# Performance work log

Hardware: AMD Instinct MI355X
Metric: run time of the kernel (lower is better)

## Reference

```python
import jax, jax.numpy as jnp
import numpy as np

DIM = 96
HEADS = 6
HEAD_DIM = DIM // HEADS
WIN = 8
N = WIN * WIN           # tokens per window
B_ = 4096               # num_windows * batch
TABLE = (2 * WIN - 1) ** 2  # 225


def setup_inputs() -> dict:
    key = jax.random.key(0)
    ks = jax.random.split(key, 7)
    x = jax.random.normal(ks[0], (B_, N, DIM), dtype=jnp.float32)
    rpi = jax.random.randint(ks[1], (N, N), 0, TABLE)
    qkv_w = jax.random.normal(ks[2], (3 * DIM, DIM), dtype=jnp.float32) * 0.02
    qkv_b = jnp.zeros((3 * DIM,), dtype=jnp.float32)
    proj_w = jax.random.normal(ks[3], (DIM, DIM), dtype=jnp.float32) * 0.02
    proj_b = jnp.zeros((DIM,), dtype=jnp.float32)
    rpb_table = jax.random.normal(ks[4], (TABLE, HEADS), dtype=jnp.float32) * 0.02
    return {"x": x, "rpi": rpi, "qkv_w": qkv_w, "qkv_b": qkv_b,
            "proj_w": proj_w, "proj_b": proj_b, "rpb_table": rpb_table}


def reference(x, rpi, qkv_w, qkv_b, proj_w, proj_b, rpb_table):
    b_, n, c = x.shape
    scale = HEAD_DIM ** -0.5
    # qkv projection: (b_, n, 3, H, hd)
    qkv = (x @ qkv_w.T + qkv_b).reshape(b_, n, 3, HEADS, HEAD_DIM)
    qkv = jnp.transpose(qkv, (2, 0, 3, 1, 4))  # (3, b_, H, n, hd)
    q, k, v = qkv[0], qkv[1], qkv[2]
    attn = jnp.einsum('bhnd,bhmd->bhnm', q * scale, k)
    # relative position bias gather: (n, n, H) -> (H, n, n)
    bias = jnp.transpose(rpb_table[rpi], (2, 0, 1))
    attn = jax.nn.softmax(attn + bias[None], axis=-1)
    out = jnp.einsum('bhnm,bhmd->bnhd', attn, v).reshape(b_, n, c)
    return out @ proj_w.T + proj_b
```

## Files before the change

kernel.cpp:

```cpp
#include <hip/hip_runtime.h>

#define NWIN 4096
#define DIM 96
#define HEADS 6
#define NTOK 64

typedef __bf16 bf16x8 __attribute__((ext_vector_type(8)));
typedef __bf16 bf16x4 __attribute__((ext_vector_type(4)));
typedef float  f32x4  __attribute__((ext_vector_type(4)));

#define WS_QKVW 0
#define WS_PROJW 55296
#define WS_BIAS 73728
#define WS_TOTAL 172032

__device__ __forceinline__ f32x4 mfma16(bf16x8 a, bf16x8 b, f32x4 c) {
  return __builtin_amdgcn_mfma_f32_16x16x32_bf16(a, b, c, 0, 0, 0);
}

__device__ __forceinline__ bf16x8 cvt8(const float* p) {
  const float4* q = (const float4*)p;
  float4 a = q[0];
  float4 b = q[1];
  bf16x8 r;
  r[0] = (__bf16)a.x; r[1] = (__bf16)a.y; r[2] = (__bf16)a.z; r[3] = (__bf16)a.w;
  r[4] = (__bf16)b.x; r[5] = (__bf16)b.y; r[6] = (__bf16)b.z; r[7] = (__bf16)b.w;
  return r;
}

__global__ void prep_kernel(const float* __restrict__ qkv_w,
                            const float* __restrict__ proj_w,
                            const float* __restrict__ rpb,
                            const int* __restrict__ rpi,
                            char* __restrict__ ws) {
  int i = blockIdx.x * blockDim.x + threadIdx.x;
  __bf16* qw = (__bf16*)(ws + WS_QKVW);
  __bf16* pw = (__bf16*)(ws + WS_PROJW);
  float* bias = (float*)(ws + WS_BIAS);
  if (i < 288 * 96) qw[i] = (__bf16)qkv_w[i];
  int j = i - 288 * 96;
  if (j >= 0 && j < 96 * 96) pw[j] = (__bf16)proj_w[j];
  int t = i - (288 * 96 + 96 * 96);
  if (t >= 0 && t < HEADS * 16 * 64 * 4) {
    int r = t & 3;
    int lane = (t >> 2) & 63;
    int ba = (t >> 8) & 15;
    int h = t >> 12;
    int bq = ba >> 2, a = ba & 3;
    int l16 = lane & 15, lq = lane >> 4;
    int qrow = 16 * bq + l16;
    int kcol = 16 * a + 4 * lq + r;
    bias[t] = rpb[rpi[qrow * 64 + kcol] * HEADS + h];
  }
}

template <bool USE_WS>
__global__ __launch_bounds__(384, 8) void win_attn(
    const float* __restrict__ x,
    const int* __restrict__ rpi,
    const float* __restrict__ qkv_w,
    const float* __restrict__ qkv_b,
    const float* __restrict__ proj_w,
    const float* __restrict__ proj_b,
    const float* __restrict__ rpb,
    const char* __restrict__ ws,
    float* __restrict__ out) {
  __shared__ __align__(16) __bf16 lds[22784];

  const int tid = (int)threadIdx.x;
  const int wv = tid >> 6;
  const int lane = tid & 63;
  const int l16 = lane & 15;
  const int lq = lane >> 4;
  const int b = (int)blockIdx.x;

  __bf16* xfrag = lds;
  __bf16* ao = lds;
  __bf16* buf = lds + 6656 + wv * 2688;
  __bf16* vh = buf + 1536;
  __bf16* Pt = vh;

  const float* xw = x + (size_t)b * (NTOK * DIM);
  const __bf16* qwb = (const __bf16*)(ws + WS_QKVW);
  const __bf16* pwb = (const __bf16*)(ws + WS_PROJW);
  const float4* bias4 = (const float4*)(ws + WS_BIAS) + (wv << 10);

  bf16x8 zf = {};

#pragma unroll
  for (int ff = 0; ff < 2; ++ff) {
    const int f = 2 * wv + ff;
    const int mt = f / 3, ks = f - 3 * mt;
    bf16x8 v = cvt8(xw + (16 * mt + l16) * DIM + 32 * ks + 8 * lq);
    *(bf16x8*)(xfrag + (f * 64 + lane) * 8) = v;
  }
  __syncthreads();

#define XV(mt, ks) (*(const bf16x8*)(xfrag + (((mt) * 3 + (ks)) * 64 + lane) * 8))

  {
    const int frow = (HEADS + wv) * 16;
    bf16x8 wb[3];
#pragma unroll
    for (int ks = 0; ks < 3; ++ks) {
      if constexpr (USE_WS)
        wb[ks] = *(const bf16x8*)(qwb + (frow + l16) * 96 + 32 * ks + 8 * lq);
      else
        wb[ks] = cvt8(qkv_w + (frow + l16) * 96 + 32 * ks + 8 * lq);
    }
    const float4 kb4 = *(const float4*)(qkv_b + frow + 4 * lq);
    const float kbv[4] = {kb4.x, kb4.y, kb4.z, kb4.w};
#pragma unroll
    for (int mt = 0; mt < 4; ++mt) {
      f32x4 acc = {0.f, 0.f, 0.f, 0.f};
#pragma unroll
      for (int ks = 0; ks < 3; ++ks) acc = mfma16(wb[ks], XV(mt, ks), acc);
      bf16x4 t;
#pragma unroll
      for (int r = 0; r < 4; ++r) t[r] = (__bf16)(acc[r] + kbv[r]);
      *(bf16x4*)(buf + (16 * mt + l16) * 24 + 4 * lq) = t;
    }
  }
  asm volatile("s_waitcnt lgkmcnt(0)" ::: "memory");

  bf16x8 kb[4];
#pragma unroll
  for (int a = 0; a < 4; ++a)
    kb[a] = (lq < 2) ? *(const bf16x8*)(buf + (16 * a + l16) * 24 + 8 * lq) : zf;

  {
    const int frow = (2 * HEADS + wv) * 16;
    bf16x8 wb[3];
#pragma unroll
    for (int ks = 0; ks < 3; ++ks) {
      if constexpr (USE_WS)
        wb[ks] = *(const bf16x8*)(qwb + (frow + l16) * 96 + 32 * ks + 8 * lq);
      else
        wb[ks] = cvt8(qkv_w + (frow + l16) * 96 + 32 * ks + 8 * lq);
    }
    const float vb = qkv_b[frow + l16];
#pragma unroll
    for (int mt = 0; mt < 4; ++mt) {
      f32x4 acc = {0.f, 0.f, 0.f, 0.f};
#pragma unroll
      for (int ks = 0; ks < 3; ++ks) acc = mfma16(XV(mt, ks), wb[ks], acc);
      bf16x4 t;
#pragma unroll
      for (int r = 0; r < 4; ++r) t[r] = (__bf16)(acc[r] + vb);
      *(bf16x4*)(vh + l16 * 72 + 16 * mt + 4 * lq) = t;
    }
  }
  asm volatile("s_waitcnt lgkmcnt(0)" ::: "memory");

  bf16x8 vbf[2];
#pragma unroll
  for (int c = 0; c < 2; ++c)
    vbf[c] = *(const bf16x8*)(vh + l16 * 72 + 32 * c + 8 * lq);

  {
    const int frow = wv * 16;
    bf16x8 wb[3];
#pragma unroll
    for (int ks = 0; ks < 3; ++ks) {
      if constexpr (USE_WS)
        wb[ks] = *(const bf16x8*)(qwb + (frow + l16) * 96 + 32 * ks + 8 * lq);
      else
        wb[ks] = cvt8(qkv_w + (frow + l16) * 96 + 32 * ks + 8 * lq);
    }
    const float4 qb4 = *(const float4*)(qkv_b + frow + 4 * lq);
    const float qbv[4] = {qb4.x, qb4.y, qb4.z, qb4.w};
#pragma unroll
    for (int mt = 0; mt < 4; ++mt) {
      f32x4 acc = {0.f, 0.f, 0.f, 0.f};
#pragma unroll
      for (int ks = 0; ks < 3; ++ks) acc = mfma16(wb[ks], XV(mt, ks), acc);
      bf16x4 t;
#pragma unroll
      for (int r = 0; r < 4; ++r) t[r] = (__bf16)((acc[r] + qbv[r]) * 0.25f);
      *(bf16x4*)(buf + (16 * mt + l16) * 24 + 4 * lq) = t;
    }
  }
#undef XV
  __syncthreads();

#pragma unroll
  for (int bq = 0; bq < 4; ++bq) {
    f32x4 s[4];
    if constexpr (USE_WS) {
#pragma unroll
      for (int a = 0; a < 4; ++a) {
        float4 t = bias4[(bq * 4 + a) * 64 + lane];
        s[a][0] = t.x; s[a][1] = t.y; s[a][2] = t.z; s[a][3] = t.w;
      }
    } else {
#pragma unroll
      for (int a = 0; a < 4; ++a)
#pragma unroll
        for (int r = 0; r < 4; ++r)
          s[a][r] = rpb[rpi[(16 * bq + l16) * 64 + 16 * a + 4 * lq + r] * HEADS + wv];
    }

    const bf16x8 qv =
        (lq < 2) ? *(const bf16x8*)(buf + (16 * bq + l16) * 24 + 8 * lq) : zf;
#pragma unroll
    for (int a = 0; a < 4; ++a) s[a] = mfma16(kb[a], qv, s[a]);

    float tp[4];
#pragma unroll
    for (int a = 0; a < 4; ++a) {
      float t0 = 0.f;
#pragma unroll
      for (int r = 0; r < 4; ++r) {
        float e = __expf(s[a][r]);
        s[a][r] = e;
        t0 += e;
      }
      tp[a] = t0;
    }
    float tsum = (tp[0] + tp[1]) + (tp[2] + tp[3]);
    tsum += __shfl_xor(tsum, 16);
    tsum += __shfl_xor(tsum, 32);
    const float rv = 1.0f / tsum;

#pragma unroll
    for (int a = 0; a < 4; ++a) {
      bf16x4 p;
#pragma unroll
      for (int r = 0; r < 4; ++r) p[r] = (__bf16)(s[a][r] * rv);
      *(bf16x4*)(Pt + l16 * 72 + 16 * a + 4 * lq) = p;
    }
    asm volatile("s_waitcnt lgkmcnt(0)" ::: "memory");

    f32x4 oacc = {0.f, 0.f, 0.f, 0.f};
#pragma unroll
    for (int c = 0; c < 2; ++c) {
      const bf16x8 pa = *(const bf16x8*)(Pt + l16 * 72 + 32 * c + 8 * lq);
      oacc = mfma16(pa, vbf[c], oacc);
    }
    asm volatile("s_waitcnt lgkmcnt(0)" ::: "memory");

#pragma unroll
    for (int r = 0; r < 4; ++r)
      ao[(16 * bq + 4 * lq + r) * 104 + 16 * wv + l16] = (__bf16)oacc[r];
  }
  __syncthreads();

  bf16x8 wpb[3];
#pragma unroll
  for (int ks = 0; ks < 3; ++ks) {
    if constexpr (USE_WS)
      wpb[ks] = *(const bf16x8*)(pwb + (16 * wv + l16) * 96 + 32 * ks + 8 * lq);
    else
      wpb[ks] = cvt8(proj_w + (16 * wv + l16) * 96 + 32 * ks + 8 * lq);
  }
  const float pb2 = proj_b[16 * wv + l16];
  float* outw = out + (size_t)b * (NTOK * DIM);
#pragma unroll
  for (int mt = 0; mt < 4; ++mt) {
    f32x4 acc = {0.f, 0.f, 0.f, 0.f};
#pragma unroll
    for (int ks = 0; ks < 3; ++ks) {
      bf16x8 aa = *(const bf16x8*)(ao + (16 * mt + l16) * 104 + 32 * ks + 8 * lq);
      acc = mfma16(aa, wpb[ks], acc);
    }
#pragma unroll
    for (int r = 0; r < 4; ++r)
      outw[(16 * mt + 4 * lq + r) * 96 + 16 * wv + l16] = acc[r] + pb2;
  }
}

extern "C" void kernel_launch(void* const* d_in, const int* in_sizes, int n_in,
                              void* d_out, int out_size, void* d_ws, size_t ws_size,
                              hipStream_t stream) {
  const float* x      = (const float*)d_in[0];
  const int*   rpi    = (const int*)d_in[1];
  const float* qkv_w  = (const float*)d_in[2];
  const float* qkv_b  = (const float*)d_in[3];
  const float* proj_w = (const float*)d_in[4];
  const float* proj_b = (const float*)d_in[5];
  const float* rpb    = (const float*)d_in[6];
  float* out = (float*)d_out;

  if (ws_size >= (size_t)WS_TOTAL) {
    prep_kernel<<<240, 256, 0, stream>>>(qkv_w, proj_w, rpb, rpi, (char*)d_ws);
    win_attn<true><<<NWIN, 384, 0, stream>>>(x, rpi, qkv_w, qkv_b, proj_w,
                                             proj_b, rpb, (const char*)d_ws, out);
  } else {
    win_attn<false><<<NWIN, 384, 0, stream>>>(x, rpi, qkv_w, qkv_b, proj_w,
                                              proj_b, rpb, (const char*)d_ws, out);
  }
}
```

Before: 86.62 us.

## Keep Q and K fragments in registers and shrink LDS footprint

Q and K are now kept in registers straight from the MFMA accumulator layout instead of being written to and re-read from LDS. The dot product over head dimensions stays correct because Q and K use the same permuted, zero-padded k-index layout. This removes the per-wave Q/K LDS buffer, which cuts shared memory per block, and the P tile gets a contiguous layout so each lane reads 8 consecutive bf16 values. The launch-bounds occupancy hint drops from 8 to 6, giving the compiler more registers to hold the extra fragments, at the cost of possible lower wave occupancy.

```diff
diff --git a/kernel.cpp b/kernel.cpp
--- a/kernel.cpp
+++ b/kernel.cpp
@@ -14,7 +14,7 @@
 #define WS_BIAS 73728
 #define WS_TOTAL 172032
 
-__device__ __forceinline__ f32x4 mfma16(bf16x8 a, bf16x8 b, f32x4 c) {
+__device__ __forceinline__ f32x4 mfma32(bf16x8 a, bf16x8 b, f32x4 c) {
   return __builtin_amdgcn_mfma_f32_16x16x32_bf16(a, b, c, 0, 0, 0);
 }
 
@@ -55,7 +55,7 @@
 }
 
 template <bool USE_WS>
-__global__ __launch_bounds__(384, 8) void win_attn(
+__global__ __launch_bounds__(384, 6) void win_attn(
     const float* __restrict__ x,
     const int* __restrict__ rpi,
     const float* __restrict__ qkv_w,
@@ -65,7 +65,7 @@
     const float* __restrict__ rpb,
     const char* __restrict__ ws,
     float* __restrict__ out) {
-  __shared__ __align__(16) __bf16 lds[22784];
+  __shared__ __align__(16) __bf16 lds[6656 + HEADS * 1152];
 
   const int tid = (int)threadIdx.x;
   const int wv = tid >> 6;
@@ -76,16 +76,13 @@
 
   __bf16* xfrag = lds;
   __bf16* ao = lds;
-  __bf16* buf = lds + 6656 + wv * 2688;
-  __bf16* vh = buf + 1536;
+  __bf16* vh = lds + 6656 + wv * 1152;
   __bf16* Pt = vh;
 
   const float* xw = x + (size_t)b * (NTOK * DIM);
   const __bf16* qwb = (const __bf16*)(ws + WS_QKVW);
   const __bf16* pwb = (const __bf16*)(ws + WS_PROJW);
   const float4* bias4 = (const float4*)(ws + WS_BIAS) + (wv << 10);
-
-  bf16x8 zf = {};
 
 #pragma unroll
   for (int ff = 0; ff < 2; ++ff) {
@@ -98,6 +95,7 @@
 
 #define XV(mt, ks) (*(const bf16x8*)(xfrag + (((mt) * 3 + (ks)) * 64 + lane) * 8))
 
+  bf16x8 kb8[4];
   {
     const int frow = (HEADS + wv) * 16;
     bf16x8 wb[3];
@@ -114,22 +112,17 @@
     for (int mt = 0; mt < 4; ++mt) {
       f32x4 acc = {0.f, 0.f, 0.f, 0.f};
 #pragma unroll
-      for (int ks = 0; ks < 3; ++ks) acc = mfma16(wb[ks], XV(mt, ks), acc);
-      bf16x4 t;
+      for (int ks = 0; ks < 3; ++ks) acc = mfma32(wb[ks], XV(mt, ks), acc);
+      bf16x8 t = {};
 #pragma unroll
       for (int r = 0; r < 4; ++r) t[r] = (__bf16)(acc[r] + kbv[r]);
-      *(bf16x4*)(buf + (16 * mt + l16) * 24 + 4 * lq) = t;
-    }
-  }
-  asm volatile("s_waitcnt lgkmcnt(0)" ::: "memory");
-
-  bf16x8 kb[4];
-#pragma unroll
-  for (int a = 0; a < 4; ++a)
-    kb[a] = (lq < 2) ? *(const bf16x8*)(buf + (16 * a + l16) * 24 + 8 * lq) : zf;
-
+      kb8[mt] = t;
+    }
+  }
+
+  bf16x4 qv4[4];
   {
-    const int frow = (2 * HEADS + wv) * 16;
+    const int frow = wv * 16;
     bf16x8 wb[3];
 #pragma unroll
     for (int ks = 0; ks < 3; ++ks) {
@@ -138,27 +131,20 @@
       else
         wb[ks] = cvt8(qkv_w + (frow + l16) * 96 + 32 * ks + 8 * lq);
     }
-    const float vb = qkv_b[frow + l16];
+    const float4 qb4 = *(const float4*)(qkv_b + frow + 4 * lq);
+    const float qbv[4] = {qb4.x, qb4.y, qb4.z, qb4.w};
 #pragma unroll
     for (int mt = 0; mt < 4; ++mt) {
       f32x4 acc = {0.f, 0.f, 0.f, 0.f};
 #pragma unroll
-      for (int ks = 0; ks < 3; ++ks) acc = mfma16(XV(mt, ks), wb[ks], acc);
-      bf16x4 t;
-#pragma unroll
-      for (int r = 0; r < 4; ++r) t[r] = (__bf16)(acc[r] + vb);
-      *(bf16x4*)(vh + l16 * 72 + 16 * mt + 4 * lq) = t;
-    }
-  }
-  asm volatile("s_waitcnt lgkmcnt(0)" ::: "memory");
-
-  bf16x8 vbf[2];
-#pragma unroll
-  for (int c = 0; c < 2; ++c)
-    vbf[c] = *(const bf16x8*)(vh + l16 * 72 + 32 * c + 8 * lq);
+      for (int ks = 0; ks < 3; ++ks) acc = mfma32(wb[ks], XV(mt, ks), acc);
+#pragma unroll
+      for (int r = 0; r < 4; ++r) qv4[mt][r] = (__bf16)((acc[r] + qbv[r]) * 0.25f);
+    }
+  }
 
   {
-    const int frow = wv * 16;
+    const int frow = (2 * HEADS + wv) * 16;
     bf16x8 wb[3];
 #pragma unroll
     for (int ks = 0; ks < 3; ++ks) {
@@ -167,20 +153,24 @@
       else
         wb[ks] = cvt8(qkv_w + (frow + l16) * 96 + 32 * ks + 8 * lq);
     }
-    const float4 qb4 = *(const float4*)(qkv_b + frow + 4 * lq);
-    const float qbv[4] = {qb4.x, qb4.y, qb4.z, qb4.w};
+    const float vb = qkv_b[frow + l16];
 #pragma unroll
     for (int mt = 0; mt < 4; ++mt) {
       f32x4 acc = {0.f, 0.f, 0.f, 0.f};
 #pragma unroll
-      for (int ks = 0; ks < 3; ++ks) acc = mfma16(wb[ks], XV(mt, ks), acc);
+      for (int ks = 0; ks < 3; ++ks) acc = mfma32(XV(mt, ks), wb[ks], acc);
       bf16x4 t;
 #pragma unroll
-      for (int r = 0; r < 4; ++r) t[r] = (__bf16)((acc[r] + qbv[r]) * 0.25f);
-      *(bf16x4*)(buf + (16 * mt + l16) * 24 + 4 * lq) = t;
-    }
-  }
-#undef XV
+      for (int r = 0; r < 4; ++r) t[r] = (__bf16)(acc[r] + vb);
+      *(bf16x4*)(vh + l16 * 72 + 16 * mt + 4 * lq) = t;
+    }
+  }
+  asm volatile("s_waitcnt lgkmcnt(0)" ::: "memory");
+  bf16x8 vbf[2];
+#pragma unroll
+  for (int c = 0; c < 2; ++c)
+    vbf[c] = *(const bf16x8*)(vh + l16 * 72 + 32 * c + 8 * lq);
+
   __syncthreads();
 
 #pragma unroll
@@ -200,10 +190,11 @@
           s[a][r] = rpb[rpi[(16 * bq + l16) * 64 + 16 * a + 4 * lq + r] * HEADS + wv];
     }
 
-    const bf16x8 qv =
-        (lq < 2) ? *(const bf16x8*)(buf + (16 * bq + l16) * 24 + 8 * lq) : zf;
-#pragma unroll
-    for (int a = 0; a < 4; ++a) s[a] = mfma16(kb[a], qv, s[a]);
+    bf16x8 q8 = {};
+#pragma unroll
+    for (int r = 0; r < 4; ++r) q8[r] = qv4[bq][r];
+#pragma unroll
+    for (int a = 0; a < 4; ++a) s[a] = mfma32(kb8[a], q8, s[a]);
 
     float tp[4];
 #pragma unroll
@@ -227,15 +218,15 @@
       bf16x4 p;
 #pragma unroll
       for (int r = 0; r < 4; ++r) p[r] = (__bf16)(s[a][r] * rv);
-      *(bf16x4*)(Pt + l16 * 72 + 16 * a + 4 * lq) = p;
+      *(bf16x4*)(Pt + (2 * a + (lq >> 1)) * 128 + l16 * 8 + (lq & 1) * 4) = p;
     }
     asm volatile("s_waitcnt lgkmcnt(0)" ::: "memory");
 
     f32x4 oacc = {0.f, 0.f, 0.f, 0.f};
 #pragma unroll
     for (int c = 0; c < 2; ++c) {
-      const bf16x8 pa = *(const bf16x8*)(Pt + l16 * 72 + 32 * c + 8 * lq);
-      oacc = mfma16(pa, vbf[c], oacc);
+      const bf16x8 pa = *(const bf16x8*)(Pt + c * 512 + lane * 8);
+      oacc = mfma32(pa, vbf[c], oacc);
     }
     asm volatile("s_waitcnt lgkmcnt(0)" ::: "memory");
 
@@ -261,7 +252,7 @@
 #pragma unroll
     for (int ks = 0; ks < 3; ++ks) {
       bf16x8 aa = *(const bf16x8*)(ao + (16 * mt + l16) * 104 + 32 * ks + 8 * lq);
-      acc = mfma16(aa, wpb[ks], acc);
+      acc = mfma32(aa, wpb[ks], acc);
     }
 #pragma unroll
     for (int r = 0; r < 4; ++r)
```

Result: slower. 102.8 us (+18.7%).
